# Kernel tuning notes

Measured on AMD Instinct MI355X. Metric: run time of the kernel, lower is better.

Reference implementation:

```python
import jax, jax.numpy as jnp
import numpy as np

B, K, H, W = 16, 256, 64, 64
TEMPERATURE = 1.0

def _build_offsets():
    # Mirrors LearnedDRoPEEnergy._build_fixed_offsets: r in {1,2} axial + diagonal,
    # then 4-neighbors (already seen) -> 16 unique offsets.
    offsets, seen = [], set()
    for r in (1, 2):
        for dy, dx in [(-r, 0), (r, 0), (0, -r), (0, r), (-r, -r), (-r, r), (r, -r), (r, r)]:
            if (dy, dx) not in seen:
                offsets.append((dy, dx)); seen.add((dy, dx))
    for dy, dx in [(-1, 0), (1, 0), (0, -1), (0, 1)]:
        if (dy, dx) not in seen:
            offsets.append((dy, dx)); seen.add((dy, dx))
    return offsets

OFFSETS = _build_offsets()

def setup_inputs() -> dict:
    key = jax.random.key(0)
    k1, k2 = jax.random.split(key)
    # Binary latent grid z in {0,1}^(B,k,H,W)
    z = jax.random.randint(k1, (B, K, H, W), 0, 2).astype(jnp.float32)
    # Per-bit importance logits (softplus'd inside reference); small random init
    w_logit = 0.1 * jax.random.normal(k2, (K,), dtype=jnp.float32)
    # Threshold init = 0.25 * k, as in LearnedHammingGate.__init__
    tau_logit = jnp.asarray(0.25 * K, dtype=jnp.float32)
    return {"z": z, "w_logit": w_logit, "tau_logit": tau_logit}

def reference(z, w_logit, tau_logit):
    # E(z; w, tau) = sum_j sum_{i in C(j)} sigmoid((tau - d_ij)/T) * d_ij
    # with d_ij = softplus(w_logit)^T (z_i XOR z_j), C(j) = 16 fixed spatial offsets.
    w = jax.nn.softplus(w_logit)                           # (k,) positive weights
    energy = jnp.zeros(z.shape[0], dtype=z.dtype)          # (B,)
    for dy, dx in OFFSETS:                                 # fixed structural loop (16)
        zs = jnp.roll(z, shift=(-dy, -dx), axis=(2, 3))    # torch.roll semantics
        xor = (z != zs).astype(z.dtype)                    # (B,k,H,W) binary XOR
        dist = jnp.einsum('bkhw,k->bhw', xor, w)           # weighted Hamming distance
        gate = jax.nn.sigmoid((tau_logit - dist) / TEMPERATURE)
        energy = energy + (gate * dist).sum(axis=(1, 2))
    return energy                                          # (B,)
```

## Files before the change

### kernel.cpp

```cpp
#include <hip/hip_runtime.h>
#include <math.h>

#define BB   16
#define KK   256
#define HWSZ 4096
#define NPOS 65536
#define NWORDS 8

__device__ __constant__ int c_dy8[8] = {-1, 0, -1, -1, -2,  0, -2, -2};
__device__ __constant__ int c_dx8[8] = { 0,-1, -1,  1,  0, -2, -2,  2};

__global__ __launch_bounds__(256) void pack_kernel(const float* __restrict__ z,
                                                   unsigned* __restrict__ pack,
                                                   float* __restrict__ out) {
    int t = blockIdx.x * 256 + threadIdx.x;
    int word = t >> 16;
    int pos  = t & (NPOS - 1);
    int b    = pos >> 12;
    int hw   = pos & (HWSZ - 1);
    const float* base = z + (size_t)(b * KK + word * 32) * HWSZ + hw;
    unsigned acc = 0u;
#pragma unroll
    for (int j = 0; j < 32; ++j) {
        float v = base[(size_t)j * HWSZ];
        acc |= (v != 0.0f) ? (1u << j) : 0u;
    }
    pack[pos * NWORDS + word] = acc;
    if (t < BB) out[t] = 0.0f;
}

__global__ __launch_bounds__(256) void energy_kernel(const unsigned* __restrict__ pack,
                                                     const float* __restrict__ w_logit,
                                                     const float* __restrict__ tau_p,
                                                     float* __restrict__ out) {
    __shared__ float wtab[32 * 256];
    __shared__ float red[4];

    int tid = threadIdx.x;
    {
        int p = tid >> 3;
        int vbase = (tid & 7) * 32;
        float wv[8];
#pragma unroll
        for (int j = 0; j < 8; ++j) {
            float x = w_logit[p * 8 + j];
            wv[j] = log1pf(expf(x));
        }
        for (int v = vbase; v < vbase + 32; ++v) {
            float s = 0.0f;
#pragma unroll
            for (int j = 0; j < 8; ++j) s += ((v >> j) & 1) ? wv[j] : 0.0f;
            wtab[p * 256 + v] = s;
        }
    }
    __syncthreads();

    float tau = tau_p[0];
    int pos = blockIdx.x * 256 + tid;
    int b = pos >> 12;
    int h = (pos >> 6) & 63;
    int w = pos & 63;

    const uint4* pk = (const uint4*)pack;
    uint4 o0 = pk[pos * 2 + 0];
    uint4 o1 = pk[pos * 2 + 1];

    float e = 0.0f;
#pragma unroll
    for (int o = 0; o < 8; ++o) {
        int h2 = (h + c_dy8[o]) & 63;
        int w2 = (w + c_dx8[o]) & 63;
        int np = (b << 12) | (h2 << 6) | w2;
        uint4 n0 = pk[np * 2 + 0];
        uint4 n1 = pk[np * 2 + 1];
        unsigned x[8];
        x[0] = o0.x ^ n0.x; x[1] = o0.y ^ n0.y; x[2] = o0.z ^ n0.z; x[3] = o0.w ^ n0.w;
        x[4] = o1.x ^ n1.x; x[5] = o1.y ^ n1.y; x[6] = o1.z ^ n1.z; x[7] = o1.w ^ n1.w;
        float d0 = 0.0f, d1 = 0.0f;
#pragma unroll
        for (int i = 0; i < 8; ++i) {
            unsigned xi = x[i];
            d0 += wtab[(i * 4 + 0) * 256 + (xi & 255)];
            d1 += wtab[(i * 4 + 1) * 256 + ((xi >> 8) & 255)];
            d0 += wtab[(i * 4 + 2) * 256 + ((xi >> 16) & 255)];
            d1 += wtab[(i * 4 + 3) * 256 + (xi >> 24)];
        }
        float d = d0 + d1;
        e += d / (1.0f + expf(d - tau));
    }

#pragma unroll
    for (int s = 32; s > 0; s >>= 1) e += __shfl_down(e, s, 64);
    int lane = tid & 63, wv = tid >> 6;
    if (lane == 0) red[wv] = e;
    __syncthreads();
    if (tid == 0) {
        float s = red[0] + red[1] + red[2] + red[3];
        atomicAdd(out + b, 2.0f * s);
    }
}

extern "C" void kernel_launch(void* const* d_in, const int* in_sizes, int n_in,
                              void* d_out, int out_size, void* d_ws, size_t ws_size,
                              hipStream_t stream) {
    const float* z       = (const float*)d_in[0];
    const float* w_logit = (const float*)d_in[1];
    const float* tau     = (const float*)d_in[2];
    float* out = (float*)d_out;
    unsigned* pack = (unsigned*)d_ws;

    hipLaunchKernelGGL(pack_kernel, dim3(NPOS * NWORDS / 256), dim3(256), 0, stream,
                       z, pack, out);
    hipLaunchKernelGGL(energy_kernel, dim3(NPOS / 256), dim3(256), 0, stream,
                       pack, w_logit, tau, out);
}
```

Measured before the change: 30.14 us.

## Repack bits into 16-bit planar words with vectorized nontemporal loads

The pack kernel now has each block handle 16 channels of one batch for all 4096 positions. Each thread reads float4 vectors with nontemporal loads and writes 16-bit packed words laid out as [b][word][hw], rather than reading strided scalars to build 32-bit words per position. The energy kernel reads these planar 16-bit words, so neighbour accesses for a given word are coalesced across adjacent positions. The cost is 16 separate short loads per neighbour where there used to be two uint4 loads, plus a smaller grid for the pack kernel.

```diff
diff --git a/kernel.cpp b/kernel.cpp
--- a/kernel.cpp
+++ b/kernel.cpp
@@ -1,35 +1,47 @@
 #include <hip/hip_runtime.h>
 #include <math.h>
 
-#define BB   16
-#define KK   256
+#define NPOS 65536
 #define HWSZ 4096
-#define NPOS 65536
-#define NWORDS 8
+
+typedef float floatx4 __attribute__((ext_vector_type(4)));
 
 __device__ __constant__ int c_dy8[8] = {-1, 0, -1, -1, -2,  0, -2, -2};
 __device__ __constant__ int c_dx8[8] = { 0,-1, -1,  1,  0, -2, -2,  2};
 
 __global__ __launch_bounds__(256) void pack_kernel(const float* __restrict__ z,
-                                                   unsigned* __restrict__ pack,
+                                                   unsigned* __restrict__ packu32,
                                                    float* __restrict__ out) {
-    int t = blockIdx.x * 256 + threadIdx.x;
-    int word = t >> 16;
-    int pos  = t & (NPOS - 1);
-    int b    = pos >> 12;
-    int hw   = pos & (HWSZ - 1);
-    const float* base = z + (size_t)(b * KK + word * 32) * HWSZ + hw;
-    unsigned acc = 0u;
+    int tid = threadIdx.x;
+    unsigned beta = blockIdx.x;
+    const float* base = z + ((size_t)beta << 16);
+    unsigned acc[16];
 #pragma unroll
-    for (int j = 0; j < 32; ++j) {
-        float v = base[(size_t)j * HWSZ];
-        acc |= (v != 0.0f) ? (1u << j) : 0u;
+    for (int t = 0; t < 16; ++t) acc[t] = 0u;
+#pragma unroll
+    for (int j = 0; j < 16; ++j) {
+#pragma unroll
+        for (int i = 0; i < 4; ++i) {
+            floatx4 v = __builtin_nontemporal_load(
+                (const floatx4*)(base + (j << 12) + (i << 10) + (tid << 2)));
+            unsigned bit = 1u << j;
+            if (v.x != 0.0f) acc[i * 4 + 0] |= bit;
+            if (v.y != 0.0f) acc[i * 4 + 1] |= bit;
+            if (v.z != 0.0f) acc[i * 4 + 2] |= bit;
+            if (v.w != 0.0f) acc[i * 4 + 3] |= bit;
+        }
     }
-    pack[pos * NWORDS + word] = acc;
-    if (t < BB) out[t] = 0.0f;
+    unsigned* dst = packu32 + ((size_t)beta << 11);
+#pragma unroll
+    for (int i = 0; i < 4; ++i) {
+        unsigned lo = acc[i * 4 + 0] | (acc[i * 4 + 1] << 16);
+        unsigned hi = acc[i * 4 + 2] | (acc[i * 4 + 3] << 16);
+        *(uint2*)(dst + (i << 9) + (tid << 1)) = make_uint2(lo, hi);
+    }
+    if (beta == 0 && tid < 16) out[tid] = 0.0f;
 }
 
-__global__ __launch_bounds__(256) void energy_kernel(const unsigned* __restrict__ pack,
+__global__ __launch_bounds__(256) void energy_kernel(const unsigned short* __restrict__ p16,
                                                      const float* __restrict__ w_logit,
                                                      const float* __restrict__ tau_p,
                                                      float* __restrict__ out) {
@@ -57,33 +69,29 @@
 
     float tau = tau_p[0];
     int pos = blockIdx.x * 256 + tid;
-    int b = pos >> 12;
-    int h = (pos >> 6) & 63;
-    int w = pos & 63;
+    int b  = pos >> 12;
+    int hw = pos & 4095;
+    int h  = hw >> 6;
+    int w  = hw & 63;
 
-    const uint4* pk = (const uint4*)pack;
-    uint4 o0 = pk[pos * 2 + 0];
-    uint4 o1 = pk[pos * 2 + 1];
+    const unsigned short* pb = p16 + ((size_t)b << 16);
+
+    unsigned cw[16];
+#pragma unroll
+    for (int q = 0; q < 16; ++q) cw[q] = pb[(q << 12) + hw];
 
     float e = 0.0f;
 #pragma unroll
     for (int o = 0; o < 8; ++o) {
         int h2 = (h + c_dy8[o]) & 63;
         int w2 = (w + c_dx8[o]) & 63;
-        int np = (b << 12) | (h2 << 6) | w2;
-        uint4 n0 = pk[np * 2 + 0];
-        uint4 n1 = pk[np * 2 + 1];
-        unsigned x[8];
-        x[0] = o0.x ^ n0.x; x[1] = o0.y ^ n0.y; x[2] = o0.z ^ n0.z; x[3] = o0.w ^ n0.w;
-        x[4] = o1.x ^ n1.x; x[5] = o1.y ^ n1.y; x[6] = o1.z ^ n1.z; x[7] = o1.w ^ n1.w;
+        int hw2 = (h2 << 6) | w2;
         float d0 = 0.0f, d1 = 0.0f;
 #pragma unroll
-        for (int i = 0; i < 8; ++i) {
-            unsigned xi = x[i];
-            d0 += wtab[(i * 4 + 0) * 256 + (xi & 255)];
-            d1 += wtab[(i * 4 + 1) * 256 + ((xi >> 8) & 255)];
-            d0 += wtab[(i * 4 + 2) * 256 + ((xi >> 16) & 255)];
-            d1 += wtab[(i * 4 + 3) * 256 + (xi >> 24)];
+        for (int q = 0; q < 16; ++q) {
+            unsigned x = cw[q] ^ (unsigned)pb[(q << 12) + hw2];
+            d0 += wtab[(2 * q + 0) * 256 + (x & 255)];
+            d1 += wtab[(2 * q + 1) * 256 + (x >> 8)];
         }
         float d = d0 + d1;
         e += d / (1.0f + expf(d - tau));
@@ -107,10 +115,10 @@
     const float* w_logit = (const float*)d_in[1];
     const float* tau     = (const float*)d_in[2];
     float* out = (float*)d_out;
-    unsigned* pack = (unsigned*)d_ws;
+    unsigned* packu32 = (unsigned*)d_ws;
 
-    hipLaunchKernelGGL(pack_kernel, dim3(NPOS * NWORDS / 256), dim3(256), 0, stream,
-                       z, pack, out);
-    hipLaunchKernelGGL(energy_kernel, dim3(NPOS / 256), dim3(256), 0, stream,
-                       pack, w_logit, tau, out);
+    hipLaunchKernelGGL(pack_kernel, dim3(256), dim3(256), 0, stream,
+                       z, packu32, out);
+    hipLaunchKernelGGL(energy_kernel, dim3(256), dim3(256), 0, stream,
+                       (const unsigned short*)packu32, w_logit, tau, out);
 }
```

Result: faster. 28.72 us (-4.7%).
